# Kernel optimization log

Measured on AMD Instinct MI355X. Metric: run time of the kernel, lower is better.

Reference implementation:

```python
import jax, jax.numpy as jnp
import numpy as np

D_MODEL = 2048
N_HEADS = 16
D_K = D_MODEL // N_HEADS
BATCH = 4
SEQ = 2048


def setup_inputs() -> dict:
    key = jax.random.key(0)
    ks = jax.random.split(key, 9)
    s = 1.0 / np.sqrt(D_MODEL)
    return {
        "x": jax.random.normal(ks[0], (BATCH, SEQ, D_MODEL), dtype=jnp.float32),
        "wq_w": jax.random.normal(ks[1], (D_MODEL, D_MODEL), dtype=jnp.float32) * s,
        "wq_b": jax.random.normal(ks[2], (D_MODEL,), dtype=jnp.float32) * 0.02,
        "wk_w": jax.random.normal(ks[3], (D_MODEL, D_MODEL), dtype=jnp.float32) * s,
        "wk_b": jax.random.normal(ks[4], (D_MODEL,), dtype=jnp.float32) * 0.02,
        "wv_w": jax.random.normal(ks[5], (D_MODEL, D_MODEL), dtype=jnp.float32) * s,
        "wv_b": jax.random.normal(ks[6], (D_MODEL,), dtype=jnp.float32) * 0.02,
        "wo_w": jax.random.normal(ks[7], (D_MODEL, D_MODEL), dtype=jnp.float32) * s,
        "wo_b": jax.random.normal(ks[8], (D_MODEL,), dtype=jnp.float32) * 0.02,
    }


def reference(x, wq_w, wq_b, wk_w, wk_b, wv_w, wv_b, wo_w, wo_b):
    b, s, _ = x.shape
    # Linear projections (torch Linear: x @ W^T + b)
    def split_heads(t):  # (b, s, d_model) -> (b, h, s, d_k)
        return t.reshape(b, s, N_HEADS, D_K).transpose(0, 2, 1, 3)
    q = split_heads(x @ wq_w.T + wq_b)
    k = split_heads(x @ wk_w.T + wk_b)
    v = split_heads(x @ wv_w.T + wv_b)
    scale = 1.0 / jnp.sqrt(jnp.asarray(D_K, dtype=x.dtype))
    scores = jnp.einsum("bhqd,bhkd->bhqk", q, k) * scale  # (b, h, s, s)
    attn = jax.nn.softmax(scores, axis=-1)
    ctx = jnp.einsum("bhqk,bhkd->bhqd", attn, v)
    ctx = ctx.transpose(0, 2, 1, 3).reshape(b, s, D_MODEL)
    out = ctx @ wo_w.T + wo_b
    return out
```

## Files before the change

### kernel.cpp

```cpp
#include <hip/hip_runtime.h>
#include <hip/hip_bf16.h>
#include <math.h>

typedef __attribute__((ext_vector_type(8))) short short8;
typedef __attribute__((ext_vector_type(4))) float f32x4;
typedef __attribute__((ext_vector_type(16))) float f32x16;
typedef __attribute__((ext_vector_type(4))) unsigned short u16x4;
typedef __attribute__((ext_vector_type(8))) unsigned short u16x8;
typedef __attribute__((ext_vector_type(4))) unsigned int u32x4;
typedef __attribute__((ext_vector_type(2))) int i32x2;
typedef unsigned short u16;
typedef unsigned int u32;

#define DM 2048
#define SQ 2048
#define NB 4
#define NH 16
#define DKH 128
#define KT 64
#define NT (SQ / KT)
#define LD3 (3 * DM)
#define NROW (NB * SQ)
#define NX8 (NROW * DM / 8)
#define NW8 (DM * DM / 8)
#define QSCALE (0.08838834764831845f * 1.4426950408889634f)

__device__ __forceinline__ u16 f2bf(float f) {
  unsigned u = __float_as_uint(f);
  u += 0x7fffu + ((u >> 16) & 1u);
  return (u16)(u >> 16);
}

__device__ __forceinline__ u32 cvtpk(float lo, float hi) {
  u32 r;
  asm("v_cvt_pk_bf16_f32 %0, %1, %2" : "=v"(r) : "v"(lo), "v"(hi));
  return r;
}

__device__ __forceinline__ void gload16(const u16* g, u16* lds) {
  __builtin_amdgcn_global_load_lds(
      (const __attribute__((address_space(1))) unsigned int*)g,
      (__attribute__((address_space(3))) unsigned int*)lds, 16, 0, 0);
}

__device__ __forceinline__ int paddr16(int r, int k, int nkt) {
  const int cid = (((r >> 8) * nkt + (k >> 6)) << 5) | (((r >> 7) & 1) << 4) |
                  (((r >> 5) & 3) << 2) | ((k >> 4) & 3);
  return (cid << 9) + (((r & 31) | (((k >> 3) & 1) << 3 << 2)) << 3) + (k & 7);
}

__device__ __forceinline__ void pinv(int idx, int nkt, int& r, int& k) {
  const int e8 = idx & 63;
  const int cid = idx >> 6;
  const int kt = (cid >> 5) % nkt;
  const int rt = (cid >> 5) / nkt;
  r = (rt << 8) + (((cid >> 4) & 1) << 7) + (((cid >> 2) & 3) << 5) + (e8 & 31);
  k = (kt << 6) + ((cid & 3) << 4) + ((e8 >> 5) << 3);
}

__global__ void cvt_all(const float* __restrict__ x,
                        const float* __restrict__ w0, const float* __restrict__ w1,
                        const float* __restrict__ w2, const float* __restrict__ w3,
                        u16* __restrict__ xb, u16* __restrict__ wqb,
                        u16* __restrict__ wob) {
  const int gid = blockIdx.x * 256 + threadIdx.x;
  const float* src;
  u16* dst;
  int idx;
  if (gid < NX8) {
    src = x; dst = xb; idx = gid;
  } else {
    const int t = gid - NX8;
    const int sel = t / NW8;
    idx = t - sel * NW8;
    src = sel == 0 ? w0 : sel == 1 ? w1 : sel == 2 ? w2 : w3;
    dst = (sel < 3) ? (wqb + (size_t)sel * DM * DM) : wob;
  }
  int r, k;
  pinv(idx, 32, r, k);
  const float4 v0 = *(const float4*)(src + (size_t)r * DM + k);
  const float4 v1 = *(const float4*)(src + (size_t)r * DM + k + 4);
  u16x8 o;
  o[0] = f2bf(v0.x); o[1] = f2bf(v0.y); o[2] = f2bf(v0.z); o[3] = f2bf(v0.w);
  o[4] = f2bf(v1.x); o[5] = f2bf(v1.y); o[6] = f2bf(v1.z); o[7] = f2bf(v1.w);
  *(u16x8*)(dst + (size_t)idx * 8) = o;
}


#define STG_A(T, HALF)                                                       \
  do {                                                                       \
    _Pragma("unroll") for (int uu = 0; uu < 2; ++uu) {                       \
      const int j_ = w * 2 + uu;                                             \
      gload16(As + ((((T) * 32 + (HALF) * 16 + j_) << 9) + l * 8),           \
              &smA[((T) & 1) * 16384 + ((HALF) * 16 + j_) * 512]);           \
    }                                                                        \
  } while (0)

#define STG_B(T, HALF)                                                       \
  do {                                                                       \
    _Pragma("unroll") for (int uu = 0; uu < 2; ++uu) {                       \
      const int j_ = w * 2 + uu;                                             \
      gload16(Bs + ((((T) * 32 + (HALF) * 16 + j_) << 9) + l * 8),           \
              &smB[((T) & 1) * 16384 + ((HALF) * 16 + j_) * 512]);           \
    }                                                                        \
  } while (0)

#define LDA(QM)                                                            \
  do {                                                                     \
    const int rb_ = wr * 4 + (QM) * 2;                                     \
    const u16* p_ = &smA[bi * 16384 + rb_ * 2048 + l * 8];                 \
    _Pragma("unroll") for (int s = 0; s < 4; ++s) {                        \
      af[0][s] = *(const short8*)&p_[s * 512];                             \
      af[1][s] = *(const short8*)&p_[2048 + s * 512];                      \
    }                                                                      \
  } while (0)

#define LDB(QN)                                                            \
  do {                                                                     \
    const int rb_ = wc * 2 + (QN);                                         \
    const u16* p_ = &smB[bi * 16384 + rb_ * 2048 + l * 8];                 \
    _Pragma("unroll") for (int s = 0; s < 4; ++s)                          \
      bf[QN][s] = *(const short8*)&p_[s * 512];                            \
  } while (0)

#define MFMA_Q(QM, QN)                                                             \
  __builtin_amdgcn_s_setprio(1);                                                   \
  _Pragma("unroll") for (int s = 0; s < 4; ++s) {                                  \
    acc[(QM) * 2][(QN)] = __builtin_amdgcn_mfma_f32_32x32x16_bf16(                 \
        af[0][s], bf[QN][s], acc[(QM) * 2][(QN)], 0, 0, 0);                        \
    acc[(QM) * 2 + 1][(QN)] = __builtin_amdgcn_mfma_f32_32x32x16_bf16(             \
        af[1][s], bf[QN][s], acc[(QM) * 2 + 1][(QN)], 0, 0, 0);                    \
  }                                                                                \
  __builtin_amdgcn_s_setprio(0);

template <int MODE>
__global__ __launch_bounds__(512, 2) void gemm8p(
    const u16* __restrict__ A, const u16* __restrict__ B,
    const float* __restrict__ bq, const float* __restrict__ bk,
    const float* __restrict__ bvp, void* __restrict__ Cout,
    int M, int N, int K) {
  __shared__ u16 smA[2 * 16384];
  __shared__ u16 smB[2 * 16384];
  const int tid = threadIdx.x;
  const int w = tid >> 6, l = tid & 63;
  const int c5 = l & 31, hi = l >> 5;
  const int wr = w >> 2, wc = w & 3;

  int flat = blockIdx.x + (int)gridDim.x * (int)blockIdx.y;
  const int nwg = (int)(gridDim.x * gridDim.y);
  flat = (flat & 7) * (nwg >> 3) + (flat >> 3);
  const int m0 = (flat / (int)gridDim.x) * 256, n0 = (flat % (int)gridDim.x) * 256;

  const int NSTEP = K / 64;
  f32x16 acc[4][2] = {};

  const u16* As = A + (size_t)(m0 >> 8) * NSTEP * 16384;
  const u16* Bs = B + (size_t)(n0 >> 8) * NSTEP * 16384;

  STG_A(0, 0); STG_A(0, 1); STG_B(0, 0); STG_B(0, 1);
  STG_B(1, 0); STG_A(1, 0);
  asm volatile("s_waitcnt vmcnt(4)" ::: "memory");
  __builtin_amdgcn_s_barrier();

  short8 af[2][4], bf[2][4];
  for (int t = 0; t < NSTEP; ++t) {
    const int bi = t & 1;
    LDA(0); LDB(0);
    if (t + 1 < NSTEP) STG_B(t + 1, 1);
    MFMA_Q(0, 0);
    __builtin_amdgcn_s_barrier();
    LDB(1);
    if (t + 1 < NSTEP) STG_A(t + 1, 1);
    MFMA_Q(0, 1);
    __builtin_amdgcn_s_barrier();
    LDA(1);
    if (t + 2 < NSTEP) STG_B(t + 2, 0);
    MFMA_Q(1, 1);
    __builtin_amdgcn_s_barrier();
    if (t + 2 < NSTEP) STG_A(t + 2, 0);
    MFMA_Q(1, 0);
    if (t + 2 < NSTEP)
      asm volatile("s_waitcnt vmcnt(4)" ::: "memory");
    else if (t + 1 < NSTEP)
      asm volatile("s_waitcnt vmcnt(0)" ::: "memory");
    __builtin_amdgcn_s_barrier();
  }

#pragma unroll
  for (int nf = 0; nf < 2; ++nf) {
    const int col = n0 + wc * 64 + nf * 32 + c5;
    float bval, os;
    if (MODE == 0) {
      const int seg = col >> 11;
      const float* bp = seg == 0 ? bq : (seg == 1 ? bk : bvp);
      bval = bp[col & (DM - 1)];
      os = (seg == 0) ? QSCALE : 1.0f;
    } else {
      bval = bq[col];
      os = 1.0f;
    }
#pragma unroll
    for (int mf = 0; mf < 4; ++mf) {
#pragma unroll
      for (int r = 0; r < 16; ++r) {
        const int row = m0 + wr * 128 + mf * 32 + (r & 3) + 8 * (r >> 2) + 4 * hi;
        const float v = (acc[mf][nf][r] + bval) * os;
        if (MODE == 1)
          ((float*)Cout)[(size_t)row * N + col] = v;
        else
          ((u16*)Cout)[(size_t)row * N + col] = f2bf(v);
      }
    }
  }
}

__global__ __launch_bounds__(512, 2) void attn(
    const u16* __restrict__ QKV, u16* __restrict__ O) {
  __shared__ u16 smK[2 * 8192];
  __shared__ u16 smV[9216];
  __shared__ float alScr[8 * 32];

  const u16* Qp = QKV;
  const u16* Kp = QKV + DM;
  const u16* Vp = QKV + 2 * DM;

  const int tid = threadIdx.x;
  const int w = tid >> 6, l = tid & 63;
  const int c5 = l & 31, hi = l >> 5;

  int flat = blockIdx.x + ((int)blockIdx.y << 3) + ((int)blockIdx.z << 7);
  flat = (flat & 7) * 64 + (flat >> 3);
  const int qt = flat & 7, h = (flat >> 3) & 15, b = flat >> 7;

  const int q0 = qt * 256 + w * 32;
  const size_t rowb = (size_t)b * SQ;
  const int hoff = h * DKH;

  short8 qf[8];
#pragma unroll
  for (int ds = 0; ds < 8; ++ds)
    qf[ds] = *(const short8*)&Qp[(rowb + q0 + c5) * LD3 + hoff + ds * 16 + hi * 8];

  f32x16 o[4] = {};
  float mrow = -1e30f, lsum = 0.f;

  const int vdg = tid >> 5;
  const int kvp = (tid & 31) * 2;
  u16x8 va, vb;

  {
#pragma unroll
    for (int uu = 0; uu < 2; ++uu) {
      const int u = w * 2 + uu;
      const int row = u * 4 + (l >> 4);
      const int col16 = (l & 15) ^ (row & 15);
      gload16(&Kp[(rowb + row) * LD3 + hoff + col16 * 8], &smK[u * 512]);
    }
    const u16* vp = &Vp[(rowb + kvp) * LD3 + hoff + vdg * 8];
    va = *(const u16x8*)vp;
    vb = *(const u16x8*)(vp + LD3);
#pragma unroll
    for (int i = 0; i < 8; ++i) {
      const int d = vdg * 8 + i;
      *(u32*)&smV[d * 72 + kvp] = (u32)va[i] | ((u32)vb[i] << 16);
    }
  }
  __syncthreads();

  int buf = 0;
  for (int t = 0; t < NT; ++t) {
    const int nb = buf ^ 1;
    if (t + 1 < NT) {
      const size_t kvr = rowb + (size_t)(t + 1) * KT;
#pragma unroll
      for (int uu = 0; uu < 2; ++uu) {
        const int u = w * 2 + uu;
        const int row = u * 4 + (l >> 4);
        const int col16 = (l & 15) ^ (row & 15);
        gload16(&Kp[(kvr + row) * LD3 + hoff + col16 * 8], &smK[nb * 8192 + u * 512]);
      }
      const u16* vp = &Vp[(kvr + kvp) * LD3 + hoff + vdg * 8];
      va = *(const u16x8*)vp;
      vb = *(const u16x8*)(vp + LD3);
    }

    f32x16 s[2] = {};
    __builtin_amdgcn_s_setprio(1);
#pragma unroll
    for (int ds = 0; ds < 8; ++ds) {
#pragma unroll
      for (int ni = 0; ni < 2; ++ni) {
        const int row = ni * 32 + c5;
        const short8 kf = *(const short8*)&smK[buf * 8192 + row * 128 + (((ds << 1) | hi) ^ (row & 15)) * 8];
        s[ni] = __builtin_amdgcn_mfma_f32_32x32x16_bf16(kf, qf[ds], s[ni], 0, 0, 0);
      }
    }
    __builtin_amdgcn_s_setprio(0);

    float mt[16];
#pragma unroll
    for (int i = 0; i < 16; ++i) mt[i] = fmaxf(s[0][i], s[1][i]);
#pragma unroll
    for (int st = 8; st >= 1; st >>= 1)
#pragma unroll
      for (int i = 0; i < st; ++i) mt[i] = fmaxf(mt[i], mt[i + st]);
    i32x2 sw = __builtin_amdgcn_permlane32_swap(__float_as_int(mt[0]), __float_as_int(mt[0]), false, false);
    const float gmax = fmaxf(__int_as_float(sw.x), __int_as_float(sw.y));

    if (__any(gmax > mrow + 10.0f)) {
      const float mn = fmaxf(mrow, gmax);
      const float al = exp2f(mrow - mn);
      mrow = mn;
      lsum *= al;
      alScr[w * 32 + c5] = al;
#pragma unroll
      for (int r = 0; r < 16; ++r) {
        const float av = alScr[w * 32 + (r & 3) + 8 * (r >> 2) + 4 * hi];
#pragma unroll
        for (int dg = 0; dg < 4; ++dg) o[dg][r] *= av;
      }
    }

    float ps0 = 0.f, ps1 = 0.f;
#pragma unroll
    for (int i = 0; i < 16; ++i) {
      const float p0 = exp2f(s[0][i] - mrow);
      const float p1 = exp2f(s[1][i] - mrow);
      s[0][i] = p0; s[1][i] = p1;
      ps0 += p0; ps1 += p1;
    }
    lsum += ps0 + ps1;

    __builtin_amdgcn_s_setprio(1);
#pragma unroll
    for (int ks = 0; ks < 4; ++ks) {
      const int b0_ = (ks & 1) * 8;
      const int ni = ks >> 1;
      const u32 A0 = cvtpk(s[ni][b0_ + 0], s[ni][b0_ + 1]);
      const u32 A1 = cvtpk(s[ni][b0_ + 4], s[ni][b0_ + 5]);
      const u32 B0 = cvtpk(s[ni][b0_ + 2], s[ni][b0_ + 3]);
      const u32 B1 = cvtpk(s[ni][b0_ + 6], s[ni][b0_ + 7]);
      const i32x2 r0 = __builtin_amdgcn_permlane32_swap((int)A0, (int)A1, false, false);
      const i32x2 r1 = __builtin_amdgcn_permlane32_swap((int)B0, (int)B1, false, false);
      u32x4 paw;
      paw.x = (u32)r0.x; paw.y = (u32)r1.x; paw.z = (u32)r0.y; paw.w = (u32)r1.y;
      const short8 pa = *(const short8*)&paw;
#pragma unroll
      for (int dg = 0; dg < 4; ++dg) {
        const int rowd = dg * 32 + c5;
        const short8 vf = *(const short8*)&smV[rowd * 72 + ks * 16 + hi * 8];
        o[dg] = __builtin_amdgcn_mfma_f32_32x32x16_bf16(pa, vf, o[dg], 0, 0, 0);
      }
    }
    __builtin_amdgcn_s_setprio(0);

    __syncthreads();
    if (t + 1 < NT) {
#pragma unroll
      for (int i = 0; i < 8; ++i) {
        const int d = vdg * 8 + i;
        *(u32*)&smV[d * 72 + kvp] = (u32)va[i] | ((u32)vb[i] << 16);
      }
      __syncthreads();
    }
    buf = nb;
  }

  {
    const i32x2 sl = __builtin_amdgcn_permlane32_swap(__float_as_int(lsum), __float_as_int(lsum), false, false);
    const float tot = __int_as_float(sl.x) + __int_as_float(sl.y);
    alScr[w * 32 + c5] = 1.0f / tot;
  }
#pragma unroll
  for (int r = 0; r < 16; ++r) {
    const int qloc = (r & 3) + 8 * (r >> 2) + 4 * hi;
    const float inv = alScr[w * 32 + qloc];
    const int rowg = (int)rowb + q0 + qloc;
#pragma unroll
    for (int dg = 0; dg < 4; ++dg)
      O[paddr16(rowg, hoff + dg * 32 + c5, 32)] = f2bf(o[dg][r] * inv);
  }
}

extern "C" void kernel_launch(void* const* d_in, const int* in_sizes, int n_in,
                              void* d_out, int out_size, void* d_ws, size_t ws_size,
                              hipStream_t stream) {
  const float* x    = (const float*)d_in[0];
  const float* wq_w = (const float*)d_in[1];
  const float* wq_b = (const float*)d_in[2];
  const float* wk_w = (const float*)d_in[3];
  const float* wk_b = (const float*)d_in[4];
  const float* wv_w = (const float*)d_in[5];
  const float* wv_b = (const float*)d_in[6];
  const float* wo_w = (const float*)d_in[7];
  const float* wo_b = (const float*)d_in[8];
  float* out = (float*)d_out;

  u16* p = (u16*)d_ws;
  u16* xb  = p; p += (size_t)NROW * DM;
  u16* wqb = p; p += (size_t)3 * DM * DM;
  u16* wob = p; p += (size_t)DM * DM;
  u16* QKV = p; p += (size_t)NROW * LD3;
  u16* ctx = xb;

  cvt_all<<<dim3((NX8 + 4 * NW8) / 256), dim3(256), 0, stream>>>(
      x, wq_w, wk_w, wv_w, wo_w, xb, wqb, wob);

  dim3 gg3(3 * DM / 256, NROW / 256);
  gemm8p<0><<<gg3, dim3(512), 0, stream>>>(xb, wqb, wq_b, wk_b, wv_b, QKV,
                                           NROW, 3 * DM, DM);

  attn<<<dim3(SQ / 256, NH, NB), dim3(512), 0, stream>>>(QKV, ctx);

  dim3 ggo(DM / 256, NROW / 256);
  gemm8p<1><<<ggo, dim3(512), 0, stream>>>(ctx, wob, wo_b, nullptr, nullptr, out,
                                           NROW, DM, DM);
}
```

Baseline: 541.2 us.

## Restructure GEMM main loop into two phases with full A-fragment preload

```diff
diff --git a/kernel.cpp b/kernel.cpp
--- a/kernel.cpp
+++ b/kernel.cpp
@@ -87,51 +87,50 @@
 }
 
 
-#define STG_A(T, HALF)                                                       \
+#define STG_AH(T, HALF)                                                      \
   do {                                                                       \
     _Pragma("unroll") for (int uu = 0; uu < 2; ++uu) {                       \
-      const int j_ = w * 2 + uu;                                             \
-      gload16(As + ((((T) * 32 + (HALF) * 16 + j_) << 9) + l * 8),           \
-              &smA[((T) & 1) * 16384 + ((HALF) * 16 + j_) * 512]);           \
+      const int j_ = (HALF) * 16 + w * 2 + uu;                               \
+      gload16(As + ((((T) * 32 + j_) << 9) + l * 8),                         \
+              &smA[((T) & 1) * 16384 + j_ * 512]);                           \
     }                                                                        \
   } while (0)
 
-#define STG_B(T, HALF)                                                       \
+#define STG_BC(T, COL)                                                       \
   do {                                                                       \
     _Pragma("unroll") for (int uu = 0; uu < 2; ++uu) {                       \
-      const int j_ = w * 2 + uu;                                             \
-      gload16(Bs + ((((T) * 32 + (HALF) * 16 + j_) << 9) + l * 8),           \
-              &smB[((T) & 1) * 16384 + ((HALF) * 16 + j_) * 512]);           \
+      const int c_ = w * 2 + uu;                                             \
+      const int j_ = ((2 * (c_ >> 2) + (COL)) << 2) + (c_ & 3);              \
+      gload16(Bs + ((((T) * 32 + j_) << 9) + l * 8),                         \
+              &smB[((T) & 1) * 16384 + j_ * 512]);                           \
     }                                                                        \
   } while (0)
 
-#define LDA(QM)                                                            \
+#define LDA_ALL                                                            \
   do {                                                                     \
-    const int rb_ = wr * 4 + (QM) * 2;                                     \
-    const u16* p_ = &smA[bi * 16384 + rb_ * 2048 + l * 8];                 \
-    _Pragma("unroll") for (int s = 0; s < 4; ++s) {                        \
-      af[0][s] = *(const short8*)&p_[s * 512];                             \
-      af[1][s] = *(const short8*)&p_[2048 + s * 512];                      \
+    _Pragma("unroll") for (int q4 = 0; q4 < 4; ++q4) {                     \
+      const u16* p_ = &smA[bi * 16384 + (wr * 4 + q4) * 2048 + l * 8];     \
+      _Pragma("unroll") for (int s = 0; s < 4; ++s)                        \
+        af[q4][s] = *(const short8*)&p_[s * 512];                          \
     }                                                                      \
   } while (0)
 
 #define LDB(QN)                                                            \
   do {                                                                     \
-    const int rb_ = wc * 2 + (QN);                                         \
-    const u16* p_ = &smB[bi * 16384 + rb_ * 2048 + l * 8];                 \
+    const u16* p_ = &smB[bi * 16384 + (wc * 2 + (QN)) * 2048 + l * 8];     \
     _Pragma("unroll") for (int s = 0; s < 4; ++s)                          \
-      bf[QN][s] = *(const short8*)&p_[s * 512];                            \
+      bf[s] = *(const short8*)&p_[s * 512];                                \
   } while (0)
 
-#define MFMA_Q(QM, QN)                                                             \
+#define MFMA_COL(QN)                                                               \
   __builtin_amdgcn_s_setprio(1);                                                   \
-  _Pragma("unroll") for (int s = 0; s < 4; ++s) {                                  \
-    acc[(QM) * 2][(QN)] = __builtin_amdgcn_mfma_f32_32x32x16_bf16(                 \
-        af[0][s], bf[QN][s], acc[(QM) * 2][(QN)], 0, 0, 0);                        \
-    acc[(QM) * 2 + 1][(QN)] = __builtin_amdgcn_mfma_f32_32x32x16_bf16(             \
-        af[1][s], bf[QN][s], acc[(QM) * 2 + 1][(QN)], 0, 0, 0);                    \
-  }                                                                                \
+  _Pragma("unroll") for (int s = 0; s < 4; ++s)                                    \
+    _Pragma("unroll") for (int q4 = 0; q4 < 4; ++q4)                               \
+      acc[q4][(QN)] = __builtin_amdgcn_mfma_f32_32x32x16_bf16(                     \
+          af[q4][s], bf[s], acc[q4][(QN)], 0, 0, 0);                               \
   __builtin_amdgcn_s_setprio(0);
+
+#define VMW(N) asm volatile("s_waitcnt vmcnt(" #N ")" ::: "memory")
 
 template <int MODE>
 __global__ __launch_bounds__(512, 2) void gemm8p(
@@ -157,32 +156,25 @@
   const u16* As = A + (size_t)(m0 >> 8) * NSTEP * 16384;
   const u16* Bs = B + (size_t)(n0 >> 8) * NSTEP * 16384;
 
-  STG_A(0, 0); STG_A(0, 1); STG_B(0, 0); STG_B(0, 1);
-  STG_B(1, 0); STG_A(1, 0);
-  asm volatile("s_waitcnt vmcnt(4)" ::: "memory");
+  STG_AH(0, 0); STG_AH(0, 1); STG_BC(0, 0); STG_BC(0, 1);
+  STG_AH(1, 0); STG_BC(1, 0);
+  VMW(4);
   __builtin_amdgcn_s_barrier();
 
-  short8 af[2][4], bf[2][4];
+  short8 af[4][4], bf[4];
   for (int t = 0; t < NSTEP; ++t) {
     const int bi = t & 1;
-    LDA(0); LDB(0);
-    if (t + 1 < NSTEP) STG_B(t + 1, 1);
-    MFMA_Q(0, 0);
+    LDA_ALL; LDB(0);
+    if (t + 1 < NSTEP) { STG_AH(t + 1, 1); STG_BC(t + 1, 1); }
+    MFMA_COL(0);
     __builtin_amdgcn_s_barrier();
     LDB(1);
-    if (t + 1 < NSTEP) STG_A(t + 1, 1);
-    MFMA_Q(0, 1);
-    __builtin_amdgcn_s_barrier();
-    LDA(1);
-    if (t + 2 < NSTEP) STG_B(t + 2, 0);
-    MFMA_Q(1, 1);
-    __builtin_amdgcn_s_barrier();
-    if (t + 2 < NSTEP) STG_A(t + 2, 0);
-    MFMA_Q(1, 0);
+    if (t + 2 < NSTEP) { STG_AH(t + 2, 0); STG_BC(t + 2, 0); }
+    MFMA_COL(1);
     if (t + 2 < NSTEP)
-      asm volatile("s_waitcnt vmcnt(4)" ::: "memory");
+      VMW(4);
     else if (t + 1 < NSTEP)
-      asm volatile("s_waitcnt vmcnt(0)" ::: "memory");
+      VMW(0);
     __builtin_amdgcn_s_barrier();
   }
 
```

New measurement: 537.7 us. No clear change (-0.6%).
